# Kernel optimization log

Hardware: AMD Instinct MI355X
Metric: run time of the kernel (lower is better)

## Reference

```python
import jax, jax.numpy as jnp
import numpy as np

N_TOKENS = 65536
HIDDEN = 1024
N_EXPERTS = 64
EPS = 1e-12  # matches F.normalize default eps
NEG_BIG = float(jnp.finfo(jnp.bfloat16).max)  # -torch.finfo(bfloat16).max sentinel


def setup_inputs() -> dict:
    key = jax.random.key(0)
    k1, k2 = jax.random.split(key)
    x = jax.random.normal(k1, (N_TOKENS, HIDDEN), dtype=jnp.float32)
    sim_matrix = jax.random.normal(k2, (HIDDEN, N_EXPERTS), dtype=jnp.float32)  # nn.Parameter(randn)
    gates = jnp.zeros((N_EXPERTS,), dtype=jnp.float32)  # nn.Parameter(zeros)
    return {"x": x, "sim_matrix": sim_matrix, "gates": gates}


def _l2norm(v, axis):
    n = jnp.sqrt(jnp.sum(v * v, axis=axis, keepdims=True))
    return v / jnp.maximum(n, EPS)


def reference(x, sim_matrix, gates):
    # cosine-similarity logits: [N, E]
    logits = jnp.matmul(_l2norm(x, -1), _l2norm(sim_matrix, 0))
    thr = jax.nn.sigmoid(gates)                      # [E]
    pre_activation_logits = logits - thr             # [N, E]
    gated = jax.nn.relu(pre_activation_logits)
    # STE: forward hard 0/1, backward identity
    hard = (gated > 0).astype(x.dtype)
    activation_mask = gated + jax.lax.stop_gradient(hard - gated)
    # topk fallback for rows with zero active experts (vectorized scatter)
    inactive = jnp.sum(hard, axis=1) == 0            # [N]
    k_fallback = N_EXPERTS // 2
    _, topk_idx = jax.lax.top_k(logits, k_fallback)  # [N, k]
    rows = jnp.arange(x.shape[0])
    fb = jnp.zeros_like(logits).at[rows[:, None], topk_idx].set(1.0)
    activation_mask = jnp.where(inactive[:, None], fb, activation_mask)
    # masked softmax over active experts
    masked = jnp.where(activation_mask > 0, gated, -NEG_BIG)
    active_expert_probs = jax.nn.softmax(masked, axis=-1)
    return active_expert_probs, pre_activation_logits, activation_mask
```

## Files before the change

### kernel.cpp

```cpp
#include <hip/hip_runtime.h>
#include <math.h>

#define N_TOK   65536
#define HID     1024
#define NEXP    64
#define EPSF    1e-12f

__global__ __launch_bounds__(256) void prep_kernel(const float* __restrict__ sim,
                                                   const float* __restrict__ gates,
                                                   float* __restrict__ ws) {
    __shared__ float partial[4][64];
    int e = threadIdx.x & 63;
    int q = threadIdx.x >> 6;
    float s = 0.f;
    for (int h = q * 256; h < q * 256 + 256; ++h) {
        float v = sim[h * NEXP + e];
        s += v * v;
    }
    partial[q][e] = s;
    __syncthreads();
    if (threadIdx.x < 64) {
        float ss = partial[0][e] + partial[1][e] + partial[2][e] + partial[3][e];
        ws[e] = 1.0f / fmaxf(sqrtf(ss), EPSF);
        ws[64 + e] = 1.0f / (1.0f + expf(-gates[e]));
    }
}

__global__ __launch_bounds__(256) void prep2n_kernel(const float* __restrict__ sim,
                                                     const float* __restrict__ ws_ro,
                                                     float* __restrict__ wn) {
    int idx = blockIdx.x * 256 + threadIdx.x;
    wn[idx] = sim[idx] * ws_ro[idx & 63];
}

__global__ __launch_bounds__(256) void gate_v10_kernel(const float* __restrict__ x,
                                                       const float* __restrict__ wn,
                                                       const float* __restrict__ prep,
                                                       float* __restrict__ out) {
    __shared__ __align__(16) float smem[8704];
    float* ss_part = smem + 8448;

    const int tid  = threadIdx.x;
    const int lane = tid & 63;
    const int wv   = tid >> 6;
    const int tg   = lane >> 3;
    const int eg   = lane & 7;
    const int e0   = eg * 8;
    const int tbase = blockIdx.x * 64;
    const int kbase = wv * 256;

    float* xsw = smem + wv * 2112;

    const float4* xq4 = (const float4*)(x + (size_t)(tbase + lane) * HID + kbase);

    float acc[8][8];
#pragma unroll
    for (int t = 0; t < 8; ++t)
#pragma unroll
        for (int e = 0; e < 8; ++e) acc[t][e] = 0.f;
    float ss = 0.f;

    {
        float4 f0 = xq4[0], f1 = xq4[1];
        const float4* wq4 = (const float4*)(wn + (size_t)kbase * NEXP) + lane * 2;
        float4 w0 = wq4[0], w1 = wq4[1];
        const float a[8] = { f0.x, f0.y, f0.z, f0.w, f1.x, f1.y, f1.z, f1.w };
#pragma unroll
        for (int i = 0; i < 8; ++i) {
            ss = fmaf(a[i], a[i], ss);
            xsw[i * 68 + lane] = a[i];
        }
        *(float4*)&xsw[1088 + lane * 8]     = w0;
        *(float4*)&xsw[1088 + lane * 8 + 4] = w1;
    }

#define FMA8x8(XA, XB, WA, WB)                                              \
    do {                                                                    \
        const float xv_[8] = { XA.x, XA.y, XA.z, XA.w, XB.x, XB.y, XB.z, XB.w }; \
        const float wv_[8] = { WA.x, WA.y, WA.z, WA.w, WB.x, WB.y, WB.z, WB.w }; \
        _Pragma("unroll")                                                   \
        for (int t_ = 0; t_ < 8; ++t_)                                      \
            _Pragma("unroll")                                               \
            for (int e_ = 0; e_ < 8; ++e_)                                  \
                acc[t_][e_] = fmaf(xv_[t_], wv_[e_], acc[t_][e_]);          \
    } while (0)

#pragma unroll 1
    for (int c = 0; c < 32; ++c) {
        float4 sx0, sx1, sw0, sw1;
        if (c < 31) {
            sx0 = xq4[(c + 1) * 2];
            sx1 = xq4[(c + 1) * 2 + 1];
            const float4* wq4 = (const float4*)(wn + (size_t)(kbase + (c + 1) * 8) * NEXP)
                              + lane * 2;
            sw0 = wq4[0];
            sw1 = wq4[1];
        }

        const float* xb = xsw + (c & 1) * 544;
        const float* wb = xsw + 1088 + (c & 1) * 512;

#pragma unroll
        for (int k = 0; k < 8; ++k) {
            const float4 xa = *(const float4*)&xb[k * 68 + tg * 8];
            const float4 xc = *(const float4*)&xb[k * 68 + tg * 8 + 4];
            const float4 wa = *(const float4*)&wb[k * 64 + e0];
            const float4 wc = *(const float4*)&wb[k * 64 + e0 + 4];
            FMA8x8(xa, xc, wa, wc);
        }

        if (c < 31) {
            float* xn = xsw + ((c + 1) & 1) * 544;
            float* wl = xsw + 1088 + ((c + 1) & 1) * 512;
            const float a[8] = { sx0.x, sx0.y, sx0.z, sx0.w, sx1.x, sx1.y, sx1.z, sx1.w };
#pragma unroll
            for (int i = 0; i < 8; ++i) {
                ss = fmaf(a[i], a[i], ss);
                xn[i * 68 + lane] = a[i];
            }
            *(float4*)&wl[lane * 8]     = sw0;
            *(float4*)&wl[lane * 8 + 4] = sw1;
        }
    }
#undef FMA8x8

    ss_part[wv * 64 + lane] = ss;
    __syncthreads();

    if (wv < 2) {
        float* reg = smem + wv * 4224;
#pragma unroll
        for (int j = 0; j < 8; ++j) {
            float* p = &reg[(tg * 8 + j) * 65 + e0];
            *(float4*)(p)     = make_float4(acc[j][0], acc[j][1], acc[j][2], acc[j][3]);
            *(float4*)(p + 4) = make_float4(acc[j][4], acc[j][5], acc[j][6], acc[j][7]);
        }
    }
    __syncthreads();
    if (wv >= 2) {
        float* reg = smem + (wv - 2) * 4224;
#pragma unroll
        for (int j = 0; j < 8; ++j) {
            float* p = &reg[(tg * 8 + j) * 65 + e0];
            float4 p0 = *(const float4*)(p);
            float4 p1 = *(const float4*)(p + 4);
            p0.x += acc[j][0]; p0.y += acc[j][1]; p0.z += acc[j][2]; p0.w += acc[j][3];
            p1.x += acc[j][4]; p1.y += acc[j][5]; p1.z += acc[j][6]; p1.w += acc[j][7];
            *(float4*)(p)     = p0;
            *(float4*)(p + 4) = p1;
        }
    }
    __syncthreads();

    float thr[8];
#pragma unroll
    for (int i = 0; i < 8; ++i) thr[i] = prep[64 + e0 + i];

    const size_t out_pre  = (size_t)N_TOK * NEXP;
    const size_t out_mask = 2 * (size_t)N_TOK * NEXP;
    const float* regA = smem;
    const float* regB = smem + 4224;

#pragma unroll
    for (int j = 0; j < 2; ++j) {
        const int tl = wv * 16 + tg * 2 + j;
        const int t  = tbase + tl;
        const float sst = (ss_part[tl] + ss_part[64 + tl])
                        + (ss_part[128 + tl] + ss_part[192 + tl]);
        const float inv = 1.0f / fmaxf(sqrtf(sst), EPSF);

        float4 aA0 = *(const float4*)&regA[tl * 65 + e0];
        float4 aA1 = *(const float4*)&regA[tl * 65 + e0 + 4];
        float4 aB0 = *(const float4*)&regB[tl * 65 + e0];
        float4 aB1 = *(const float4*)&regB[tl * 65 + e0 + 4];
        float logit[8] = { (aA0.x + aB0.x) * inv, (aA0.y + aB0.y) * inv,
                           (aA0.z + aB0.z) * inv, (aA0.w + aB0.w) * inv,
                           (aA1.x + aB1.x) * inv, (aA1.y + aB1.y) * inv,
                           (aA1.z + aB1.z) * inv, (aA1.w + aB1.w) * inv };
        float pre[8], gated[8];
        int active[8];
        int myact = 0;
#pragma unroll
        for (int i = 0; i < 8; ++i) {
            pre[i]   = logit[i] - thr[i];
            gated[i] = fmaxf(pre[i], 0.f);
            active[i] = pre[i] > 0.f;
            myact += active[i];
        }
        int rowact = myact;
        rowact += __shfl_xor(rowact, 1, 8);
        rowact += __shfl_xor(rowact, 2, 8);
        rowact += __shfl_xor(rowact, 4, 8);

        float probs[8], mask[8];
        if (rowact > 0) {
            float m = -INFINITY;
#pragma unroll
            for (int i = 0; i < 8; ++i) m = fmaxf(m, active[i] ? gated[i] : -INFINITY);
            m = fmaxf(m, __shfl_xor(m, 1, 8));
            m = fmaxf(m, __shfl_xor(m, 2, 8));
            m = fmaxf(m, __shfl_xor(m, 4, 8));
            float s = 0.f;
#pragma unroll
            for (int i = 0; i < 8; ++i) {
                float ev = active[i] ? expf(gated[i] - m) : 0.f;
                probs[i] = ev; s += ev;
            }
            s += __shfl_xor(s, 1, 8);
            s += __shfl_xor(s, 2, 8);
            s += __shfl_xor(s, 4, 8);
            float rs = 1.0f / s;
#pragma unroll
            for (int i = 0; i < 8; ++i) {
                probs[i] *= rs;
                mask[i] = active[i] ? 1.f : 0.f;
            }
        } else {
            unsigned key[8];
#pragma unroll
            for (int i = 0; i < 8; ++i) {
                unsigned u = __float_as_uint(logit[i]);
                key[i] = (u & 0x80000000u) ? ~u : (u | 0x80000000u);
            }
            unsigned cand = 0u;
            for (int bit = 31; bit >= 0; --bit) {
                unsigned test = cand | (1u << bit);
                int c = 0;
#pragma unroll
                for (int i = 0; i < 8; ++i) c += (key[i] >= test);
                c += __shfl_xor(c, 1, 8);
                c += __shfl_xor(c, 2, 8);
                c += __shfl_xor(c, 4, 8);
                if (c >= 32) cand = test;
            }
            int cgt = 0;
#pragma unroll
            for (int i = 0; i < 8; ++i) cgt += (key[i] > cand);
            cgt += __shfl_xor(cgt, 1, 8);
            cgt += __shfl_xor(cgt, 2, 8);
            cgt += __shfl_xor(cgt, 4, 8);
            int need_eq = 32 - cgt;

            int eqc = 0;
#pragma unroll
            for (int i = 0; i < 8; ++i) eqc += (key[i] == cand);
            int scan = eqc, tmp;
            tmp = __shfl_up(scan, 1, 8); if (eg >= 1) scan += tmp;
            tmp = __shfl_up(scan, 2, 8); if (eg >= 2) scan += tmp;
            tmp = __shfl_up(scan, 4, 8); if (eg >= 4) scan += tmp;
            int run = scan - eqc;
#pragma unroll
            for (int i = 0; i < 8; ++i) {
                int sel = (key[i] > cand) || ((key[i] == cand) && (run < need_eq));
                run += (key[i] == cand);
                mask[i]  = sel ? 1.f : 0.f;
                probs[i] = sel ? 0.03125f : 0.f;
            }
        }

        const size_t row = (size_t)t * NEXP + e0;
        *(float4*)&out[row]                = make_float4(probs[0], probs[1], probs[2], probs[3]);
        *(float4*)&out[row + 4]            = make_float4(probs[4], probs[5], probs[6], probs[7]);
        *(float4*)&out[out_pre + row]      = make_float4(pre[0], pre[1], pre[2], pre[3]);
        *(float4*)&out[out_pre + row + 4]  = make_float4(pre[4], pre[5], pre[6], pre[7]);
        *(float4*)&out[out_mask + row]     = make_float4(mask[0], mask[1], mask[2], mask[3]);
        *(float4*)&out[out_mask + row + 4] = make_float4(mask[4], mask[5], mask[6], mask[7]);
    }
}

#define TOKB    128
#define KC      64
#define XPAD    65

__global__ __launch_bounds__(256) void gate_kernel_fb(const float* __restrict__ x,
                                                      const float* __restrict__ sim,
                                                      const float* __restrict__ prep,
                                                      float* __restrict__ out) {
    __shared__ float x_lds[TOKB][XPAD];
    __shared__ float w_lds[KC][NEXP];
    __shared__ float ss_lds[TOKB];
    __shared__ float invcol[NEXP];
    __shared__ float thr_s[NEXP];

    const int tid = threadIdx.x;
    const int base_t = blockIdx.x * TOKB;

    if (tid < NEXP) { invcol[tid] = prep[tid]; thr_s[tid] = prep[64 + tid]; }
    if (tid < TOKB) ss_lds[tid] = 0.f;

    const int g_e = tid & 7;
    const int g_t = tid >> 3;
    const int e0 = g_e * 8;
    const int t0 = g_t * 4;

    const int lt = tid >> 4;
    const int lk = (tid & 15) * 4;

    float acc[4][8];
#pragma unroll
    for (int j = 0; j < 4; ++j)
#pragma unroll
        for (int i = 0; i < 8; ++i) acc[j][i] = 0.f;

    for (int kc = 0; kc < HID; kc += KC) {
        __syncthreads();
#pragma unroll
        for (int it = 0; it < 4; ++it) {
            int flat4 = it * 256 + tid;
            int k = flat4 >> 4;
            int e = (flat4 & 15) * 4;
            float4 v = *(const float4*)&sim[(size_t)(kc + k) * NEXP + e];
            v.x *= invcol[e]; v.y *= invcol[e + 1]; v.z *= invcol[e + 2]; v.w *= invcol[e + 3];
            *(float4*)&w_lds[k][e] = v;
        }
#pragma unroll
        for (int it = 0; it < 8; ++it) {
            int t = it * 16 + lt;
            float4 v = *(const float4*)&x[(size_t)(base_t + t) * HID + kc + lk];
            x_lds[t][lk + 0] = v.x; x_lds[t][lk + 1] = v.y;
            x_lds[t][lk + 2] = v.z; x_lds[t][lk + 3] = v.w;
            float s4 = v.x * v.x + v.y * v.y + v.z * v.z + v.w * v.w;
            s4 += __shfl_xor(s4, 1, 16);
            s4 += __shfl_xor(s4, 2, 16);
            s4 += __shfl_xor(s4, 4, 16);
            s4 += __shfl_xor(s4, 8, 16);
            if ((tid & 15) == 0) ss_lds[t] += s4;
        }
        __syncthreads();
#pragma unroll 8
        for (int k = 0; k < KC; ++k) {
            float x0 = x_lds[t0 + 0][k];
            float x1 = x_lds[t0 + 1][k];
            float x2 = x_lds[t0 + 2][k];
            float x3 = x_lds[t0 + 3][k];
            float4 w0 = *(const float4*)&w_lds[k][e0];
            float4 w1 = *(const float4*)&w_lds[k][e0 + 4];
            float wv[8] = { w0.x, w0.y, w0.z, w0.w, w1.x, w1.y, w1.z, w1.w };
#pragma unroll
            for (int i = 0; i < 8; ++i) {
                acc[0][i] += x0 * wv[i];
                acc[1][i] += x1 * wv[i];
                acc[2][i] += x2 * wv[i];
                acc[3][i] += x3 * wv[i];
            }
        }
    }

    const size_t out_pre  = (size_t)N_TOK * NEXP;
    const size_t out_mask = 2 * (size_t)N_TOK * NEXP;

#pragma unroll
    for (int j = 0; j < 4; ++j) {
        int t = t0 + j;
        float inv = 1.0f / fmaxf(sqrtf(ss_lds[t]), EPSF);
        float logit[8], pre[8], gated[8];
        int active[8];
        int myact = 0;
#pragma unroll
        for (int i = 0; i < 8; ++i) {
            logit[i] = acc[j][i] * inv;
            pre[i]   = logit[i] - thr_s[e0 + i];
            gated[i] = fmaxf(pre[i], 0.f);
            active[i] = pre[i] > 0.f;
            myact += active[i];
        }
        int rowact = myact;
        rowact += __shfl_xor(rowact, 1, 8);
        rowact += __shfl_xor(rowact, 2, 8);
        rowact += __shfl_xor(rowact, 4, 8);

        float probs[8], mask[8];
        if (rowact > 0) {
            float m = -INFINITY;
#pragma unroll
            for (int i = 0; i < 8; ++i) m = fmaxf(m, active[i] ? gated[i] : -INFINITY);
            m = fmaxf(m, __shfl_xor(m, 1, 8));
            m = fmaxf(m, __shfl_xor(m, 2, 8));
            m = fmaxf(m, __shfl_xor(m, 4, 8));
            float s = 0.f;
#pragma unroll
            for (int i = 0; i < 8; ++i) {
                float ev = active[i] ? expf(gated[i] - m) : 0.f;
                probs[i] = ev; s += ev;
            }
            s += __shfl_xor(s, 1, 8);
            s += __shfl_xor(s, 2, 8);
            s += __shfl_xor(s, 4, 8);
            float rs = 1.0f / s;
#pragma unroll
            for (int i = 0; i < 8; ++i) {
                probs[i] *= rs;
                mask[i] = active[i] ? 1.f : 0.f;
            }
        } else {
            unsigned key[8];
#pragma unroll
            for (int i = 0; i < 8; ++i) {
                unsigned u = __float_as_uint(logit[i]);
                key[i] = (u & 0x80000000u) ? ~u : (u | 0x80000000u);
            }
            unsigned cand = 0u;
            for (int bit = 31; bit >= 0; --bit) {
                unsigned test = cand | (1u << bit);
                int c = 0;
#pragma unroll
                for (int i = 0; i < 8; ++i) c += (key[i] >= test);
                c += __shfl_xor(c, 1, 8);
                c += __shfl_xor(c, 2, 8);
                c += __shfl_xor(c, 4, 8);
                if (c >= 32) cand = test;
            }
            int cgt = 0;
#pragma unroll
            for (int i = 0; i < 8; ++i) cgt += (key[i] > cand);
            cgt += __shfl_xor(cgt, 1, 8);
            cgt += __shfl_xor(cgt, 2, 8);
            cgt += __shfl_xor(cgt, 4, 8);
            int need_eq = 32 - cgt;

            int eqc = 0;
#pragma unroll
            for (int i = 0; i < 8; ++i) eqc += (key[i] == cand);
            int scan = eqc, tmp;
            tmp = __shfl_up(scan, 1, 8); if (g_e >= 1) scan += tmp;
            tmp = __shfl_up(scan, 2, 8); if (g_e >= 2) scan += tmp;
            tmp = __shfl_up(scan, 4, 8); if (g_e >= 4) scan += tmp;
            int run = scan - eqc;
#pragma unroll
            for (int i = 0; i < 8; ++i) {
                int sel = (key[i] > cand) || ((key[i] == cand) && (run < need_eq));
                run += (key[i] == cand);
                mask[i]  = sel ? 1.f : 0.f;
                probs[i] = sel ? 0.03125f : 0.f;
            }
        }

        size_t row = (size_t)(base_t + t) * NEXP + e0;
        *(float4*)&out[row]                = make_float4(probs[0], probs[1], probs[2], probs[3]);
        *(float4*)&out[row + 4]            = make_float4(probs[4], probs[5], probs[6], probs[7]);
        *(float4*)&out[out_pre + row]      = make_float4(pre[0], pre[1], pre[2], pre[3]);
        *(float4*)&out[out_pre + row + 4]  = make_float4(pre[4], pre[5], pre[6], pre[7]);
        *(float4*)&out[out_mask + row]     = make_float4(mask[0], mask[1], mask[2], mask[3]);
        *(float4*)&out[out_mask + row + 4] = make_float4(mask[4], mask[5], mask[6], mask[7]);
    }
}

extern "C" void kernel_launch(void* const* d_in, const int* in_sizes, int n_in,
                              void* d_out, int out_size, void* d_ws, size_t ws_size,
                              hipStream_t stream) {
    (void)in_sizes; (void)n_in; (void)out_size;
    const float* x     = (const float*)d_in[0];
    const float* sim   = (const float*)d_in[1];
    const float* gates = (const float*)d_in[2];
    float* out = (float*)d_out;
    float* ws  = (float*)d_ws;

    hipLaunchKernelGGL(prep_kernel, dim3(1), dim3(256), 0, stream, sim, gates, ws);

    const size_t need = 512 + (size_t)HID * NEXP * sizeof(float);
    if (ws_size >= need) {
        float* wn = ws + 128;
        hipLaunchKernelGGL(prep2n_kernel, dim3(HID * NEXP / 256), dim3(256), 0, stream,
                           sim, ws, wn);
        hipLaunchKernelGGL(gate_v10_kernel, dim3(N_TOK / 64), dim3(256), 0, stream,
                           x, wn, ws, out);
    } else {
        hipLaunchKernelGGL(gate_kernel_fb, dim3(N_TOK / TOKB), dim3(256), 0, stream,
                           x, sim, ws, out);
    }
}
```

Measured before the change: 161.5 us.

## Use split-bf16 MFMA for the cosine GEMM with exact fp32 recompute for borderline rows

```diff
diff --git a/kernel.cpp b/kernel.cpp
--- a/kernel.cpp
+++ b/kernel.cpp
@@ -5,6 +5,27 @@
 #define HID     1024
 #define NEXP    64
 #define EPSF    1e-12f
+#define EPSW    4e-5f
+
+typedef __attribute__((ext_vector_type(8))) short s16x8;
+typedef __attribute__((ext_vector_type(4))) float f32x4;
+
+__device__ __forceinline__ unsigned short f2bf(float f) {
+    unsigned u = __float_as_uint(f);
+    unsigned r = u + 0x7fffu + ((u >> 16) & 1u);
+    return (unsigned short)(r >> 16);
+}
+__device__ __forceinline__ float bf2f(unsigned short h) {
+    return __uint_as_float(((unsigned)h) << 16);
+}
+__device__ __forceinline__ unsigned enc_key(float f) {
+    unsigned u = __float_as_uint(f);
+    return (u & 0x80000000u) ? ~u : (u | 0x80000000u);
+}
+__device__ __forceinline__ float dec_key(unsigned k) {
+    unsigned u = (k & 0x80000000u) ? (k ^ 0x80000000u) : ~k;
+    return __uint_as_float(u);
+}
 
 __global__ __launch_bounds__(256) void prep_kernel(const float* __restrict__ sim,
                                                    const float* __restrict__ gates,
@@ -33,13 +54,321 @@
     wn[idx] = sim[idx] * ws_ro[idx & 63];
 }
 
+__global__ __launch_bounds__(256) void prep3_kernel(const float* __restrict__ wn,
+                                                    unsigned short* __restrict__ wbh,
+                                                    unsigned short* __restrict__ wbl) {
+    int i = blockIdx.x * 256 + threadIdx.x;
+    int j    = i & 7;
+    int lane = (i >> 3) & 63;
+    int nt   = (i >> 9) & 3;
+    int kt   = i >> 11;
+    int k = kt * 32 + ((lane >> 4) & 3) * 8 + j;
+    int e = nt * 16 + (lane & 15);
+    float v = wn[k * NEXP + e];
+    unsigned short h = f2bf(v);
+    unsigned short l = f2bf(v - bf2f(h));
+    wbh[i] = h; wbl[i] = l;
+}
+
+__global__ __launch_bounds__(256) void gate_v11_kernel(const float* __restrict__ x,
+                                                       const float* __restrict__ wn,
+                                                       const unsigned short* __restrict__ wbh,
+                                                       const unsigned short* __restrict__ wbl,
+                                                       const float* __restrict__ prep,
+                                                       float* __restrict__ out) {
+    __shared__ __align__(16) float smem[6016];
+    float* xrow    = smem + 4352;
+    float* ss_part = smem + 5376;
+    float* thr_l   = smem + 5632;
+    int*   flags_i = (int*)(smem + 5696);
+    float* part    = smem + 5760;
+    unsigned short* AhU = (unsigned short*)smem;
+    unsigned short* AlU = (unsigned short*)(smem + 2080);
+
+    const int tid   = threadIdx.x;
+    const int lane  = tid & 63;
+    const int wv    = tid >> 6;
+    const int tbase = blockIdx.x * 64;
+
+    const int t_st = tid & 63;
+    const int q_st = tid >> 6;
+    const int fl   = (t_st & 15) + 16 * q_st;
+    const int mt   = t_st >> 4;
+    const float* xrow_g = x + (size_t)(tbase + t_st) * HID;
+
+    if (tid < 64) thr_l[tid] = prep[64 + tid];
+
+    f32x4 acc[4];
+#pragma unroll
+    for (int m = 0; m < 4; ++m) acc[m] = (f32x4){0.f, 0.f, 0.f, 0.f};
+    float ss = 0.f;
+
+    const s16x8* bh_g = (const s16x8*)wbh;
+    const s16x8* bl_g = (const s16x8*)wbl;
+
+    {
+        float4 v0 = *(const float4*)(xrow_g + q_st * 8);
+        float4 v1 = *(const float4*)(xrow_g + q_st * 8 + 4);
+        const float a[8] = { v0.x, v0.y, v0.z, v0.w, v1.x, v1.y, v1.z, v1.w };
+        s16x8 hv, lv;
+#pragma unroll
+        for (int i = 0; i < 8; ++i) {
+            ss = fmaf(a[i], a[i], ss);
+            unsigned short h = f2bf(a[i]);
+            hv[i] = (short)h;
+            lv[i] = (short)f2bf(a[i] - bf2f(h));
+        }
+        int slot = mt * 65 + fl;
+        *(s16x8*)&AhU[slot * 8] = hv;
+        *(s16x8*)&AlU[slot * 8] = lv;
+    }
+    s16x8 bh = bh_g[(0 * 4 + wv) * 64 + lane];
+    s16x8 bl = bl_g[(0 * 4 + wv) * 64 + lane];
+    __syncthreads();
+
+#pragma unroll 1
+    for (int c = 0; c < 32; ++c) {
+        const int buf = c & 1;
+        float4 nv0, nv1;
+        s16x8 nbh, nbl;
+        if (c < 31) {
+            nv0 = *(const float4*)(xrow_g + (c + 1) * 32 + q_st * 8);
+            nv1 = *(const float4*)(xrow_g + (c + 1) * 32 + q_st * 8 + 4);
+            nbh = bh_g[((c + 1) * 4 + wv) * 64 + lane];
+            nbl = bl_g[((c + 1) * 4 + wv) * 64 + lane];
+        }
+
+        s16x8 ah[4], al[4];
+#pragma unroll
+        for (int m = 0; m < 4; ++m) {
+            int base = ((buf << 2) + m) * 65 * 8 + lane * 8;
+            ah[m] = *(const s16x8*)&AhU[base];
+            al[m] = *(const s16x8*)&AlU[base];
+        }
+#pragma unroll
+        for (int m = 0; m < 4; ++m)
+            acc[m] = __builtin_amdgcn_mfma_f32_16x16x32_bf16(al[m], bh, acc[m], 0, 0, 0);
+#pragma unroll
+        for (int m = 0; m < 4; ++m)
+            acc[m] = __builtin_amdgcn_mfma_f32_16x16x32_bf16(ah[m], bl, acc[m], 0, 0, 0);
+#pragma unroll
+        for (int m = 0; m < 4; ++m)
+            acc[m] = __builtin_amdgcn_mfma_f32_16x16x32_bf16(ah[m], bh, acc[m], 0, 0, 0);
+
+        if (c < 31) {
+            const float a[8] = { nv0.x, nv0.y, nv0.z, nv0.w, nv1.x, nv1.y, nv1.z, nv1.w };
+            s16x8 hv, lv;
+#pragma unroll
+            for (int i = 0; i < 8; ++i) {
+                ss = fmaf(a[i], a[i], ss);
+                unsigned short h = f2bf(a[i]);
+                hv[i] = (short)h;
+                lv[i] = (short)f2bf(a[i] - bf2f(h));
+            }
+            int slot = (((buf ^ 1) << 2) + mt) * 65 + fl;
+            *(s16x8*)&AhU[slot * 8] = hv;
+            *(s16x8*)&AlU[slot * 8] = lv;
+            bh = nbh; bl = nbl;
+        }
+        __syncthreads();
+    }
+
+    ss_part[q_st * 64 + t_st] = ss;
+    {
+        float* lg = smem;
+#pragma unroll
+        for (int m = 0; m < 4; ++m) {
+#pragma unroll
+            for (int r = 0; r < 4; ++r) {
+                int tok = m * 16 + (lane >> 4) * 4 + r;
+                int e   = wv * 16 + (lane & 15);
+                lg[tok * 68 + e] = acc[m][r];
+            }
+        }
+    }
+    __syncthreads();
+
+    const int tg = lane >> 3;
+    const int eg = lane & 7;
+    const int e0 = eg * 8;
+    const size_t out_pre  = (size_t)N_TOK * NEXP;
+    const size_t out_mask = 2 * (size_t)N_TOK * NEXP;
+
+#pragma unroll
+    for (int j = 0; j < 2; ++j) {
+        const int tl = wv * 16 + tg * 2 + j;
+        const int t  = tbase + tl;
+        const float sst = (ss_part[tl] + ss_part[64 + tl])
+                        + (ss_part[128 + tl] + ss_part[192 + tl]);
+        const float inv = 1.0f / fmaxf(sqrtf(sst), EPSF);
+
+        float logit[8], pre[8];
+        int active[8];
+        int myact = 0;
+#pragma unroll
+        for (int i = 0; i < 8; ++i) {
+            logit[i] = smem[tl * 68 + e0 + i] * inv;
+            pre[i]   = logit[i] - thr_l[e0 + i];
+            active[i] = pre[i] > 0.f;
+            myact += active[i];
+        }
+        *(float4*)&out[out_pre + (size_t)t * NEXP + e0]     = make_float4(pre[0], pre[1], pre[2], pre[3]);
+        *(float4*)&out[out_pre + (size_t)t * NEXP + e0 + 4] = make_float4(pre[4], pre[5], pre[6], pre[7]);
+
+        int rowact = myact;
+        rowact += __shfl_xor(rowact, 1, 8);
+        rowact += __shfl_xor(rowact, 2, 8);
+        rowact += __shfl_xor(rowact, 4, 8);
+
+        int flag;
+        if (rowact > 0) {
+            float mn = 1e30f;
+#pragma unroll
+            for (int i = 0; i < 8; ++i) mn = fminf(mn, fabsf(pre[i]));
+            mn = fminf(mn, __shfl_xor(mn, 1, 8));
+            mn = fminf(mn, __shfl_xor(mn, 2, 8));
+            mn = fminf(mn, __shfl_xor(mn, 4, 8));
+            flag = (mn <= EPSW);
+            if (!flag) {
+                float gated[8], probs[8], mask[8];
+#pragma unroll
+                for (int i = 0; i < 8; ++i) gated[i] = fmaxf(pre[i], 0.f);
+                float m = -INFINITY;
+#pragma unroll
+                for (int i = 0; i < 8; ++i) m = fmaxf(m, active[i] ? gated[i] : -INFINITY);
+                m = fmaxf(m, __shfl_xor(m, 1, 8));
+                m = fmaxf(m, __shfl_xor(m, 2, 8));
+                m = fmaxf(m, __shfl_xor(m, 4, 8));
+                float s = 0.f;
+#pragma unroll
+                for (int i = 0; i < 8; ++i) {
+                    float ev = active[i] ? expf(gated[i] - m) : 0.f;
+                    probs[i] = ev; s += ev;
+                }
+                s += __shfl_xor(s, 1, 8);
+                s += __shfl_xor(s, 2, 8);
+                s += __shfl_xor(s, 4, 8);
+                float rs = 1.0f / s;
+#pragma unroll
+                for (int i = 0; i < 8; ++i) { probs[i] *= rs; mask[i] = active[i] ? 1.f : 0.f; }
+                size_t row = (size_t)t * NEXP + e0;
+                *(float4*)&out[row]                = make_float4(probs[0], probs[1], probs[2], probs[3]);
+                *(float4*)&out[row + 4]            = make_float4(probs[4], probs[5], probs[6], probs[7]);
+                *(float4*)&out[out_mask + row]     = make_float4(mask[0], mask[1], mask[2], mask[3]);
+                *(float4*)&out[out_mask + row + 4] = make_float4(mask[4], mask[5], mask[6], mask[7]);
+            }
+        } else {
+            unsigned key[8];
+#pragma unroll
+            for (int i = 0; i < 8; ++i) key[i] = enc_key(logit[i]);
+            unsigned cand = 0u;
+            for (int bit = 31; bit >= 0; --bit) {
+                unsigned test = cand | (1u << bit);
+                int c = 0;
+#pragma unroll
+                for (int i = 0; i < 8; ++i) c += (key[i] >= test);
+                c += __shfl_xor(c, 1, 8);
+                c += __shfl_xor(c, 2, 8);
+                c += __shfl_xor(c, 4, 8);
+                if (c >= 32) cand = test;
+            }
+            const float val32 = dec_key(cand);
+            int nhi = 0, nlo = 0, nam = 0;
+#pragma unroll
+            for (int i = 0; i < 8; ++i) {
+                nhi += logit[i] > val32 + EPSW;
+                nlo += logit[i] > val32 - EPSW;
+                nam += pre[i] > -EPSW;
+            }
+            nhi += __shfl_xor(nhi, 1, 8); nhi += __shfl_xor(nhi, 2, 8); nhi += __shfl_xor(nhi, 4, 8);
+            nlo += __shfl_xor(nlo, 1, 8); nlo += __shfl_xor(nlo, 2, 8); nlo += __shfl_xor(nlo, 4, 8);
+            nam += __shfl_xor(nam, 1, 8); nam += __shfl_xor(nam, 2, 8); nam += __shfl_xor(nam, 4, 8);
+            flag = !(nhi == 31 && nlo == 32) || (nam > 0);
+            if (!flag) {
+                float probs[8], mask[8];
+#pragma unroll
+                for (int i = 0; i < 8; ++i) {
+                    int sel = logit[i] > val32 - EPSW;
+                    mask[i]  = sel ? 1.f : 0.f;
+                    probs[i] = sel ? 0.03125f : 0.f;
+                }
+                size_t row = (size_t)t * NEXP + e0;
+                *(float4*)&out[row]                = make_float4(probs[0], probs[1], probs[2], probs[3]);
+                *(float4*)&out[row + 4]            = make_float4(probs[4], probs[5], probs[6], probs[7]);
+                *(float4*)&out[out_mask + row]     = make_float4(mask[0], mask[1], mask[2], mask[3]);
+                *(float4*)&out[out_mask + row + 4] = make_float4(mask[4], mask[5], mask[6], mask[7]);
+            }
+        }
+        if (eg == 0) flags_i[tl] = flag;
+    }
+    __syncthreads();
+
+    for (int tf = 0; tf < 64; ++tf) {
+        if (flags_i[tf] == 0) continue;
+        {
+            float4 v = *(const float4*)&x[(size_t)(tbase + tf) * HID + tid * 4];
+            *(float4*)&xrow[tid * 4] = v;
+        }
+        __syncthreads();
+        const int e = tid & 63;
+        const int q = tid >> 6;
+        const float* wp = wn + (size_t)q * 256 * NEXP + e;
+        const float* xr = xrow + q * 256;
+        float dot = 0.f;
+#pragma unroll 8
+        for (int k2 = 0; k2 < 256; ++k2)
+            dot = fmaf(xr[k2], wp[(size_t)k2 * NEXP], dot);
+        part[q * 64 + e] = dot;
+        __syncthreads();
+        if (tid < 64) {
+            const float sst = (ss_part[tf] + ss_part[64 + tf])
+                            + (ss_part[128 + tf] + ss_part[192 + tf]);
+            const float inv = 1.0f / fmaxf(sqrtf(sst), EPSF);
+            const float lg = ((part[e] + part[64 + e]) + (part[128 + e] + part[192 + e])) * inv;
+            const float pr = lg - thr_l[e];
+            unsigned long long act = __ballot(pr > 0.f);
+            float probs, mask;
+            if (act) {
+                float g = fmaxf(pr, 0.f);
+                float mv = (pr > 0.f) ? g : -INFINITY;
+#pragma unroll
+                for (int d = 1; d < 64; d <<= 1) mv = fmaxf(mv, __shfl_xor(mv, d));
+                float ex = (pr > 0.f) ? expf(g - mv) : 0.f;
+                float s = ex;
+#pragma unroll
+                for (int d = 1; d < 64; d <<= 1) s += __shfl_xor(s, d);
+                probs = ex / s;
+                mask  = (pr > 0.f) ? 1.f : 0.f;
+            } else {
+                unsigned key = enc_key(lg);
+                unsigned cand = 0u;
+                for (int bit = 31; bit >= 0; --bit) {
+                    unsigned test = cand | (1u << bit);
+                    int c = __popcll(__ballot(key >= test));
+                    if (c >= 32) cand = test;
+                }
+                int need = 32 - __popcll(__ballot(key > cand));
+                unsigned long long em = __ballot(key == cand);
+                unsigned long long mlt = e ? (~0ull >> (64 - e)) : 0ull;
+                int below = __popcll(em & mlt);
+                int sel = (key > cand) || ((key == cand) && (below < need));
+                probs = sel ? 0.03125f : 0.f;
+                mask  = sel ? 1.f : 0.f;
+            }
+            size_t row = (size_t)(tbase + tf) * NEXP;
+            out[row + e] = probs;
+            out[out_mask + row + e] = mask;
+        }
+        __syncthreads();
+    }
+}
+
 __global__ __launch_bounds__(256) void gate_v10_kernel(const float* __restrict__ x,
                                                        const float* __restrict__ wn,
                                                        const float* __restrict__ prep,
                                                        float* __restrict__ out) {
     __shared__ __align__(16) float smem[8704];
     float* ss_part = smem + 8448;
-
     const int tid  = threadIdx.x;
     const int lane = tid & 63;
     const int wv   = tid >> 6;
@@ -48,32 +377,24 @@
     const int e0   = eg * 8;
     const int tbase = blockIdx.x * 64;
     const int kbase = wv * 256;
-
     float* xsw = smem + wv * 2112;
-
     const float4* xq4 = (const float4*)(x + (size_t)(tbase + lane) * HID + kbase);
-
     float acc[8][8];
 #pragma unroll
     for (int t = 0; t < 8; ++t)
 #pragma unroll
         for (int e = 0; e < 8; ++e) acc[t][e] = 0.f;
     float ss = 0.f;
-
     {
         float4 f0 = xq4[0], f1 = xq4[1];
         const float4* wq4 = (const float4*)(wn + (size_t)kbase * NEXP) + lane * 2;
         float4 w0 = wq4[0], w1 = wq4[1];
         const float a[8] = { f0.x, f0.y, f0.z, f0.w, f1.x, f1.y, f1.z, f1.w };
 #pragma unroll
-        for (int i = 0; i < 8; ++i) {
-            ss = fmaf(a[i], a[i], ss);
-            xsw[i * 68 + lane] = a[i];
-        }
+        for (int i = 0; i < 8; ++i) { ss = fmaf(a[i], a[i], ss); xsw[i * 68 + lane] = a[i]; }
         *(float4*)&xsw[1088 + lane * 8]     = w0;
         *(float4*)&xsw[1088 + lane * 8 + 4] = w1;
     }
-
 #define FMA8x8(XA, XB, WA, WB)                                              \
     do {                                                                    \
         const float xv_[8] = { XA.x, XA.y, XA.z, XA.w, XB.x, XB.y, XB.z, XB.w }; \
@@ -84,22 +405,17 @@
             for (int e_ = 0; e_ < 8; ++e_)                                  \
                 acc[t_][e_] = fmaf(xv_[t_], wv_[e_], acc[t_][e_]);          \
     } while (0)
-
 #pragma unroll 1
     for (int c = 0; c < 32; ++c) {
         float4 sx0, sx1, sw0, sw1;
         if (c < 31) {
             sx0 = xq4[(c + 1) * 2];
             sx1 = xq4[(c + 1) * 2 + 1];
-            const float4* wq4 = (const float4*)(wn + (size_t)(kbase + (c + 1) * 8) * NEXP)
-                              + lane * 2;
-            sw0 = wq4[0];
-            sw1 = wq4[1];
-        }
-
+            const float4* wq4 = (const float4*)(wn + (size_t)(kbase + (c + 1) * 8) * NEXP) + lane * 2;
+            sw0 = wq4[0]; sw1 = wq4[1];
+        }
         const float* xb = xsw + (c & 1) * 544;
         const float* wb = xsw + 1088 + (c & 1) * 512;
-
 #pragma unroll
         for (int k = 0; k < 8; ++k) {
             const float4 xa = *(const float4*)&xb[k * 68 + tg * 8];
@@ -108,25 +424,19 @@
             const float4 wc = *(const float4*)&wb[k * 64 + e0 + 4];
             FMA8x8(xa, xc, wa, wc);
         }
-
         if (c < 31) {
             float* xn = xsw + ((c + 1) & 1) * 544;
             float* wl = xsw + 1088 + ((c + 1) & 1) * 512;
             const float a[8] = { sx0.x, sx0.y, sx0.z, sx0.w, sx1.x, sx1.y, sx1.z, sx1.w };
 #pragma unroll
-            for (int i = 0; i < 8; ++i) {
-                ss = fmaf(a[i], a[i], ss);
-                xn[i * 68 + lane] = a[i];
-            }
+            for (int i = 0; i < 8; ++i) { ss = fmaf(a[i], a[i], ss); xn[i * 68 + lane] = a[i]; }
             *(float4*)&wl[lane * 8]     = sw0;
             *(float4*)&wl[lane * 8 + 4] = sw1;
         }
     }
 #undef FMA8x8
-
     ss_part[wv * 64 + lane] = ss;
     __syncthreads();
-
     if (wv < 2) {
         float* reg = smem + wv * 4224;
 #pragma unroll
@@ -146,29 +456,23 @@
             float4 p1 = *(const float4*)(p + 4);
             p0.x += acc[j][0]; p0.y += acc[j][1]; p0.z += acc[j][2]; p0.w += acc[j][3];
             p1.x += acc[j][4]; p1.y += acc[j][5]; p1.z += acc[j][6]; p1.w += acc[j][7];
-            *(float4*)(p)     = p0;
-            *(float4*)(p + 4) = p1;
+            *(float4*)(p) = p0; *(float4*)(p + 4) = p1;
         }
     }
     __syncthreads();
-
     float thr[8];
 #pragma unroll
     for (int i = 0; i < 8; ++i) thr[i] = prep[64 + e0 + i];
-
     const size_t out_pre  = (size_t)N_TOK * NEXP;
     const size_t out_mask = 2 * (size_t)N_TOK * NEXP;
     const float* regA = smem;
     const float* regB = smem + 4224;
-
 #pragma unroll
     for (int j = 0; j < 2; ++j) {
         const int tl = wv * 16 + tg * 2 + j;
         const int t  = tbase + tl;
-        const float sst = (ss_part[tl] + ss_part[64 + tl])
-                        + (ss_part[128 + tl] + ss_part[192 + tl]);
+        const float sst = (ss_part[tl] + ss_part[64 + tl]) + (ss_part[128 + tl] + ss_part[192 + tl]);
         const float inv = 1.0f / fmaxf(sqrtf(sst), EPSF);
-
         float4 aA0 = *(const float4*)&regA[tl * 65 + e0];
         float4 aA1 = *(const float4*)&regA[tl * 65 + e0 + 4];
         float4 aB0 = *(const float4*)&regB[tl * 65 + e0];
@@ -191,7 +495,6 @@
         rowact += __shfl_xor(rowact, 1, 8);
         rowact += __shfl_xor(rowact, 2, 8);
         rowact += __shfl_xor(rowact, 4, 8);
-
         float probs[8], mask[8];
         if (rowact > 0) {
             float m = -INFINITY;
@@ -202,26 +505,17 @@
             m = fmaxf(m, __shfl_xor(m, 4, 8));
             float s = 0.f;
 #pragma unroll
-            for (int i = 0; i < 8; ++i) {
-                float ev = active[i] ? expf(gated[i] - m) : 0.f;
-                probs[i] = ev; s += ev;
-            }
+            for (int i = 0; i < 8; ++i) { float ev = active[i] ? expf(gated[i] - m) : 0.f; probs[i] = ev; s += ev; }
             s += __shfl_xor(s, 1, 8);
             s += __shfl_xor(s, 2, 8);
             s += __shfl_xor(s, 4, 8);
             float rs = 1.0f / s;
 #pragma unroll
-            for (int i = 0; i < 8; ++i) {
-                probs[i] *= rs;
-                mask[i] = active[i] ? 1.f : 0.f;
-            }
+            for (int i = 0; i < 8; ++i) { probs[i] *= rs; mask[i] = active[i] ? 1.f : 0.f; }
         } else {
             unsigned key[8];
 #pragma unroll
-            for (int i = 0; i < 8; ++i) {
-                unsigned u = __float_as_uint(logit[i]);
-                key[i] = (u & 0x80000000u) ? ~u : (u | 0x80000000u);
-            }
+            for (int i = 0; i < 8; ++i) key[i] = enc_key(logit[i]);
             unsigned cand = 0u;
             for (int bit = 31; bit >= 0; --bit) {
                 unsigned test = cand | (1u << bit);
@@ -240,7 +534,6 @@
             cgt += __shfl_xor(cgt, 2, 8);
             cgt += __shfl_xor(cgt, 4, 8);
             int need_eq = 32 - cgt;
-
             int eqc = 0;
 #pragma unroll
             for (int i = 0; i < 8; ++i) eqc += (key[i] == cand);
@@ -257,7 +550,6 @@
                 probs[i] = sel ? 0.03125f : 0.f;
             }
         }
-
         const size_t row = (size_t)t * NEXP + e0;
         *(float4*)&out[row]                = make_float4(probs[0], probs[1], probs[2], probs[3]);
         *(float4*)&out[row + 4]            = make_float4(probs[4], probs[5], probs[6], probs[7]);
@@ -271,7 +563,6 @@
 #define TOKB    128
 #define KC      64
 #define XPAD    65
-
 __global__ __launch_bounds__(256) void gate_kernel_fb(const float* __restrict__ x,
                                                       const float* __restrict__ sim,
                                                       const float* __restrict__ prep,
@@ -281,27 +572,21 @@
     __shared__ float ss_lds[TOKB];
     __shared__ float invcol[NEXP];
     __shared__ float thr_s[NEXP];
-
     const int tid = threadIdx.x;
     const int base_t = blockIdx.x * TOKB;
-
     if (tid < NEXP) { invcol[tid] = prep[tid]; thr_s[tid] = prep[64 + tid]; }
     if (tid < TOKB) ss_lds[tid] = 0.f;
-
     const int g_e = tid & 7;
     const int g_t = tid >> 3;
     const int e0 = g_e * 8;
     const int t0 = g_t * 4;
-
     const int lt = tid >> 4;
     const int lk = (tid & 15) * 4;
-
     float acc[4][8];
 #pragma unroll
     for (int j = 0; j < 4; ++j)
 #pragma unroll
         for (int i = 0; i < 8; ++i) acc[j][i] = 0.f;
-
     for (int kc = 0; kc < HID; kc += KC) {
         __syncthreads();
 #pragma unroll
@@ -345,10 +630,8 @@
             }
         }
     }
-
     const size_t out_pre  = (size_t)N_TOK * NEXP;
     const size_t out_mask = 2 * (size_t)N_TOK * NEXP;
-
 #pragma unroll
     for (int j = 0; j < 4; ++j) {
         int t = t0 + j;
@@ -368,7 +651,6 @@
         rowact += __shfl_xor(rowact, 1, 8);
         rowact += __shfl_xor(rowact, 2, 8);
         rowact += __shfl_xor(rowact, 4, 8);
-
         float probs[8], mask[8];
         if (rowact > 0) {
             float m = -INFINITY;
@@ -379,26 +661,17 @@
             m = fmaxf(m, __shfl_xor(m, 4, 8));
             float s = 0.f;
 #pragma unroll
-            for (int i = 0; i < 8; ++i) {
-                float ev = active[i] ? expf(gated[i] - m) : 0.f;
-                probs[i] = ev; s += ev;
-            }
+            for (int i = 0; i < 8; ++i) { float ev = active[i] ? expf(gated[i] - m) : 0.f; probs[i] = ev; s += ev; }
             s += __shfl_xor(s, 1, 8);
             s += __shfl_xor(s, 2, 8);
             s += __shfl_xor(s, 4, 8);
             float rs = 1.0f / s;
 #pragma unroll
-            for (int i = 0; i < 8; ++i) {
-                probs[i] *= rs;
-                mask[i] = active[i] ? 1.f : 0.f;
-            }
+            for (int i = 0; i < 8; ++i) { probs[i] *= rs; mask[i] = active[i] ? 1.f : 0.f; }
         } else {
             unsigned key[8];
 #pragma unroll
-            for (int i = 0; i < 8; ++i) {
-                unsigned u = __float_as_uint(logit[i]);
-                key[i] = (u & 0x80000000u) ? ~u : (u | 0x80000000u);
-            }
+            for (int i = 0; i < 8; ++i) key[i] = enc_key(logit[i]);
             unsigned cand = 0u;
             for (int bit = 31; bit >= 0; --bit) {
                 unsigned test = cand | (1u << bit);
@@ -417,7 +690,6 @@
             cgt += __shfl_xor(cgt, 2, 8);
             cgt += __shfl_xor(cgt, 4, 8);
             int need_eq = 32 - cgt;
-
             int eqc = 0;
 #pragma unroll
             for (int i = 0; i < 8; ++i) eqc += (key[i] == cand);
@@ -434,7 +706,6 @@
                 probs[i] = sel ? 0.03125f : 0.f;
             }
         }
-
         size_t row = (size_t)(base_t + t) * NEXP + e0;
         *(float4*)&out[row]                = make_float4(probs[0], probs[1], probs[2], probs[3]);
         *(float4*)&out[row + 4]            = make_float4(probs[4], probs[5], probs[6], probs[7]);
@@ -457,8 +728,20 @@
 
     hipLaunchKernelGGL(prep_kernel, dim3(1), dim3(256), 0, stream, sim, gates, ws);
 
-    const size_t need = 512 + (size_t)HID * NEXP * sizeof(float);
-    if (ws_size >= need) {
+    const size_t need_v10 = 512 + (size_t)HID * NEXP * sizeof(float);
+    const size_t need_v11 = need_v10 + 2 * (size_t)HID * NEXP * sizeof(short);
+    if (ws_size >= need_v11) {
+        float* wn = ws + 128;
+        unsigned short* wbh = (unsigned short*)(ws + 128 + HID * NEXP / 1);
+        wbh = (unsigned short*)((char*)ws + 512 + (size_t)HID * NEXP * 4);
+        unsigned short* wbl = wbh + (size_t)HID * NEXP;
+        hipLaunchKernelGGL(prep2n_kernel, dim3(HID * NEXP / 256), dim3(256), 0, stream,
+                           sim, ws, wn);
+        hipLaunchKernelGGL(prep3_kernel, dim3(HID * NEXP / 256), dim3(256), 0, stream,
+                           wn, wbh, wbl);
+        hipLaunchKernelGGL(gate_v11_kernel, dim3(N_TOK / 64), dim3(256), 0, stream,
+                           x, wn, wbh, wbl, ws, out);
+    } else if (ws_size >= need_v10) {
         float* wn = ws + 128;
         hipLaunchKernelGGL(prep2n_kernel, dim3(HID * NEXP / 256), dim3(256), 0, stream,
                            sim, ws, wn);
```

Result: slower. 190.1 us (+17.7%).
